# Performance work log

Measured on AMD Instinct MI355X. Metric: run time of the kernel, lower is better.

## Reference

```python
import jax, jax.numpy as jnp
import numpy as np

def setup_inputs() -> dict:
    key = jax.random.key(0)
    k0, k1, k2, k3 = jax.random.split(key, 4)
    B, L, D, E, Dg = 2, 2048, 2048, 8, 256  # Dg = D // E
    x = jax.random.normal(k0, (B, L, D), dtype=jnp.float32)
    Wg = jax.random.normal(k1, (E, D), dtype=jnp.float32) * 0.02     # gate: Linear(D, E)
    Wd = jax.random.normal(k2, (E, Dg, D), dtype=jnp.float32) * 0.02  # down: Linear(D, Dg) per expert
    Wu = jax.random.normal(k3, (E, D, Dg), dtype=jnp.float32) * 0.02  # up:   Linear(Dg, D) per expert
    return {"x": x, "Wg": Wg, "Wd": Wd, "Wu": Wu, "k": 2}

def reference(x, Wg, Wd, Wu, k):
    B, L, D = x.shape
    E = Wg.shape[0]
    T = B * L
    xf = x.reshape(T, D)
    # gate scores: sigmoid(x @ Wg^T), then top-k gate values G and expert indices I
    S = jax.nn.sigmoid(xf @ Wg.T)            # [T, E]
    G, I = jax.lax.top_k(S, k)               # [T, k], [T, k]
    # combine weights per token per expert (zero for unselected experts);
    # equivalent to the original's one_hot + per-expert gather/scatter-add.
    w = jnp.zeros((T, E), x.dtype).at[jnp.arange(T)[:, None], I].add(G)  # [T, E]
    # down: sum_e w[t,e] * (Wd[e] @ x[t])
    down = jnp.einsum('te,egd,td->tg', w, Wd, xf)   # [T, Dg]
    # inner model is identity
    # up: sum_e w[t,e] * (Wu[e] @ down[t])
    up = jnp.einsum('te,edg,tg->td', w, Wu, down)   # [T, D]
    return up.reshape(B, L, D)
```

## Files before the change

kernel.cpp:

```cpp
#include <hip/hip_runtime.h>
#include <stdint.h>

#define T_TOK 4096
#define DIM   2048
#define NEXP  8
#define DG    256
#define TOPK  2

#define BM 64
#define BN 128
#define BKU 64
#define NROWS  (T_TOK*TOPK + NEXP*BM)
#define NBLK_M (NROWS/BM)

typedef __attribute__((ext_vector_type(8))) short short8;
typedef __attribute__((ext_vector_type(4))) float f32x4;

static __device__ __forceinline__ short f2bf(float f) {
    union { float f; uint32_t u; } v{f};
    uint32_t r = v.u + 0x7fffu + ((v.u >> 16) & 1u);
    return (short)(r >> 16);
}
static __device__ __forceinline__ float b2f(short s) {
    union { uint32_t u; float f; } v{((uint32_t)(unsigned short)s) << 16};
    return v.f;
}

#define GLD16(g, l) \
    __builtin_amdgcn_global_load_lds((const __attribute__((address_space(1))) void*)(g), \
                                     (__attribute__((address_space(3))) void*)(l), 16, 0, 0)

__global__ __launch_bounds__(256) void gate_kernel(const float* __restrict__ x,
                                                   const float* __restrict__ Wg,
                                                   int* __restrict__ gidx,
                                                   float* __restrict__ gval,
                                                   short* __restrict__ x_bf)
{
    int token = blockIdx.x * 4 + (threadIdx.x >> 6);
    int lane  = threadIdx.x & 63;
    const float4* xr = (const float4*)(x + (size_t)token * DIM);

    float4 xv[8];
#pragma unroll
    for (int i = 0; i < 8; i++) xv[i] = xr[lane + 64 * i];

    short4* xb = (short4*)(x_bf + (size_t)token * DIM);
#pragma unroll
    for (int i = 0; i < 8; i++) {
        short4 o;
        o.x = f2bf(xv[i].x); o.y = f2bf(xv[i].y);
        o.z = f2bf(xv[i].z); o.w = f2bf(xv[i].w);
        xb[lane + 64 * i] = o;
    }

    float acc[NEXP];
#pragma unroll
    for (int e = 0; e < NEXP; e++) {
        const float4* wr = (const float4*)(Wg + e * DIM);
        float a = 0.0f;
#pragma unroll
        for (int i = 0; i < 8; i++) {
            float4 w = wr[lane + 64 * i];
            a += xv[i].x * w.x + xv[i].y * w.y + xv[i].z * w.z + xv[i].w * w.w;
        }
        acc[e] = a;
    }

#pragma unroll
    for (int m = 1; m < 64; m <<= 1) {
#pragma unroll
        for (int e = 0; e < NEXP; e++) acc[e] += __shfl_xor(acc[e], m, 64);
    }

    if (lane == 0) {
        float sg[NEXP];
#pragma unroll
        for (int e = 0; e < NEXP; e++) sg[e] = 1.0f / (1.0f + expf(-acc[e]));
        int i0 = 0;
#pragma unroll
        for (int e = 1; e < NEXP; e++) if (sg[e] > sg[i0]) i0 = e;
        int i1 = (i0 == 0) ? 1 : 0;
#pragma unroll
        for (int e = 0; e < NEXP; e++) if (e != i0 && e != i1 && sg[e] > sg[i1]) i1 = e;
        gidx[2 * token + 0] = i0;
        gidx[2 * token + 1] = i1;
        gval[2 * token + 0] = sg[i0];
        gval[2 * token + 1] = sg[i1];
    }
}

__global__ __launch_bounds__(256) void convW_kernel(const float* __restrict__ Wd,
                                                    const float* __restrict__ Wu,
                                                    short* __restrict__ Wd_bf,
                                                    short* __restrict__ Wu_bf,
                                                    int n4)
{
    int i = blockIdx.x * 256 + threadIdx.x;
    const float* s; short* d; int j;
    if (i < n4)      { s = Wd; d = Wd_bf; j = i; }
    else             { s = Wu; d = Wu_bf; j = i - n4; if (j >= n4) return; }
    float4 v = ((const float4*)s)[j];
    short4 o;
    o.x = f2bf(v.x); o.y = f2bf(v.y); o.z = f2bf(v.z); o.w = f2bf(v.w);
    ((short4*)d)[j] = o;
}

__global__ __launch_bounds__(1024) void bucket_kernel(const int* __restrict__ gidx,
                                                      int* __restrict__ rowtok,
                                                      int* __restrict__ rowpos,
                                                      int* __restrict__ seg_off)
{
    __shared__ int cnt[NEXP];
    __shared__ int cur[NEXP];
    int tid = threadIdx.x;
    if (tid < NEXP) cnt[tid] = 0;
    __syncthreads();

    for (int t = tid; t < T_TOK; t += 1024) {
        atomicAdd(&cnt[gidx[2 * t + 0]], 1);
        atomicAdd(&cnt[gidx[2 * t + 1]], 1);
    }
    __syncthreads();

    if (tid == 0) {
        int o = 0;
        for (int e = 0; e < NEXP; e++) {
            seg_off[e] = o;
            cur[e] = o;
            o += ((cnt[e] + BM - 1) / BM) * BM;
        }
        seg_off[NEXP] = o;
    }
    __syncthreads();

    for (int r = tid; r < NROWS; r += 1024) rowtok[r] = -1;
    __syncthreads();

    for (int t = tid; t < T_TOK; t += 1024) {
        for (int s = 0; s < TOPK; s++) {
            int e = gidx[2 * t + s];
            int p = atomicAdd(&cur[e], 1);
            rowtok[p] = t;
            rowpos[2 * t + s] = p;
        }
    }
}

#define AS3 __attribute__((address_space(3)))

#define STAGE(B_) do { \
    GLD16(agA0, lA_##B_##_0); \
    GLD16(agA1, lA_##B_##_1); \
    GLD16(agB0, lB_##B_##_0); \
    GLD16(agB1, lB_##B_##_1); \
    GLD16(agB2, lB_##B_##_2); \
    GLD16(agB3, lB_##B_##_3); \
    agA0 += BKU; agA1 += BKU; \
    agB0 += BKU; agB1 += BKU; agB2 += BKU; agB3 += BKU; \
} while (0)

#define COMP(B_) do { \
    short8 a00 = *(const short8*)&As[B_][am0][c0]; \
    short8 a10 = *(const short8*)&As[B_][am1][c0]; \
    short8 b00 = *(const short8*)&Bs[B_][bn0][c0]; \
    short8 b10 = *(const short8*)&Bs[B_][bn1][c0]; \
    short8 b20 = *(const short8*)&Bs[B_][bn2][c0]; \
    short8 b30 = *(const short8*)&Bs[B_][bn3][c0]; \
    short8 a01 = *(const short8*)&As[B_][am0][c1]; \
    short8 a11 = *(const short8*)&As[B_][am1][c1]; \
    short8 b01 = *(const short8*)&Bs[B_][bn0][c1]; \
    short8 b11 = *(const short8*)&Bs[B_][bn1][c1]; \
    short8 b21 = *(const short8*)&Bs[B_][bn2][c1]; \
    short8 b31 = *(const short8*)&Bs[B_][bn3][c1]; \
    acc[0][0] = __builtin_amdgcn_mfma_f32_16x16x32_bf16(a00, b00, acc[0][0], 0, 0, 0); \
    acc[0][1] = __builtin_amdgcn_mfma_f32_16x16x32_bf16(a00, b10, acc[0][1], 0, 0, 0); \
    acc[0][2] = __builtin_amdgcn_mfma_f32_16x16x32_bf16(a00, b20, acc[0][2], 0, 0, 0); \
    acc[0][3] = __builtin_amdgcn_mfma_f32_16x16x32_bf16(a00, b30, acc[0][3], 0, 0, 0); \
    acc[1][0] = __builtin_amdgcn_mfma_f32_16x16x32_bf16(a10, b00, acc[1][0], 0, 0, 0); \
    acc[1][1] = __builtin_amdgcn_mfma_f32_16x16x32_bf16(a10, b10, acc[1][1], 0, 0, 0); \
    acc[1][2] = __builtin_amdgcn_mfma_f32_16x16x32_bf16(a10, b20, acc[1][2], 0, 0, 0); \
    acc[1][3] = __builtin_amdgcn_mfma_f32_16x16x32_bf16(a10, b30, acc[1][3], 0, 0, 0); \
    acc[0][0] = __builtin_amdgcn_mfma_f32_16x16x32_bf16(a01, b01, acc[0][0], 0, 0, 0); \
    acc[0][1] = __builtin_amdgcn_mfma_f32_16x16x32_bf16(a01, b11, acc[0][1], 0, 0, 0); \
    acc[0][2] = __builtin_amdgcn_mfma_f32_16x16x32_bf16(a01, b21, acc[0][2], 0, 0, 0); \
    acc[0][3] = __builtin_amdgcn_mfma_f32_16x16x32_bf16(a01, b31, acc[0][3], 0, 0, 0); \
    acc[1][0] = __builtin_amdgcn_mfma_f32_16x16x32_bf16(a11, b01, acc[1][0], 0, 0, 0); \
    acc[1][1] = __builtin_amdgcn_mfma_f32_16x16x32_bf16(a11, b11, acc[1][1], 0, 0, 0); \
    acc[1][2] = __builtin_amdgcn_mfma_f32_16x16x32_bf16(a11, b21, acc[1][2], 0, 0, 0); \
    acc[1][3] = __builtin_amdgcn_mfma_f32_16x16x32_bf16(a11, b31, acc[1][3], 0, 0, 0); \
} while (0)

template<int K, int Ntot>
__global__ __launch_bounds__(256) void gemm_kernel(const short* __restrict__ A,
                                                   const short* __restrict__ B,
                                                   const int* __restrict__ rowtok,
                                                   const int* __restrict__ seg_off,
                                                   short* __restrict__ C)
{
    __shared__ __align__(16) short As[2][BM][BKU];
    __shared__ __align__(16) short Bs[2][BN][BKU];

    int row0 = blockIdx.x * BM;
    int total = seg_off[NEXP];
    if (row0 >= total) return;
    int e = 0;
    while (row0 >= seg_off[e + 1]) ++e;
    int n0 = blockIdx.y * BN;

    int tid = threadIdx.x;
    int w = tid >> 6, l = tid & 63;

    int srow = (w << 3) + (l >> 3);
    int sc   = ((l & 7) ^ ((l >> 3) & 7)) << 3;

    int ta0 = rowtok[row0 + srow];      if (ta0 < 0) ta0 = 0;
    int ta1 = rowtok[row0 + 32 + srow]; if (ta1 < 0) ta1 = 0;
    const short* agA0 = A + (size_t)ta0 * K + sc;
    const short* agA1 = A + (size_t)ta1 * K + sc;
    const short* be = B + (size_t)e * Ntot * K + (size_t)n0 * K;
    const short* agB0 = be + (size_t)(srow     ) * K + sc;
    const short* agB1 = be + (size_t)(srow + 32) * K + sc;
    const short* agB2 = be + (size_t)(srow + 64) * K + sc;
    const short* agB3 = be + (size_t)(srow + 96) * K + sc;

    auto lA_0_0 = (AS3 void*)&As[0][(w << 3)     ][0];
    auto lA_0_1 = (AS3 void*)&As[0][(w << 3) + 32][0];
    auto lA_1_0 = (AS3 void*)&As[1][(w << 3)     ][0];
    auto lA_1_1 = (AS3 void*)&As[1][(w << 3) + 32][0];
    auto lB_0_0 = (AS3 void*)&Bs[0][(w << 3)     ][0];
    auto lB_0_1 = (AS3 void*)&Bs[0][(w << 3) + 32][0];
    auto lB_0_2 = (AS3 void*)&Bs[0][(w << 3) + 64][0];
    auto lB_0_3 = (AS3 void*)&Bs[0][(w << 3) + 96][0];
    auto lB_1_0 = (AS3 void*)&Bs[1][(w << 3)     ][0];
    auto lB_1_1 = (AS3 void*)&Bs[1][(w << 3) + 32][0];
    auto lB_1_2 = (AS3 void*)&Bs[1][(w << 3) + 64][0];
    auto lB_1_3 = (AS3 void*)&Bs[1][(w << 3) + 96][0];

    int mlane = l & 15, qlane = l >> 4;
    int wm = w >> 1, wn = w & 1;
    int c0 = (qlane ^ (mlane & 7)) << 3;
    int c1 = c0 ^ 32;
    int am0 = wm * 32 + mlane, am1 = am0 + 16;
    int bn0 = wn * 64 + mlane, bn1 = bn0 + 16, bn2 = bn0 + 32, bn3 = bn0 + 48;

    f32x4 acc[2][4] = {};

    STAGE(0);
    __syncthreads();
    constexpr int NT = K / BKU;
#pragma unroll 1
    for (int t = 0; t < NT; t += 2) {
        if (t + 1 < NT) STAGE(1);
        COMP(0);
        __syncthreads();
        if (t + 2 < NT) STAGE(0);
        COMP(1);
        __syncthreads();
    }

#pragma unroll
    for (int i = 0; i < 2; i++) {
        int rbase = row0 + wm * 32 + i * 16 + qlane * 4;
#pragma unroll
        for (int j = 0; j < 4; j++) {
            int col = n0 + wn * 64 + j * 16 + mlane;
#pragma unroll
            for (int r = 0; r < 4; r++)
                C[(size_t)(rbase + r) * Ntot + col] = f2bf(acc[i][j][r]);
        }
    }
}

#undef STAGE
#undef COMP
#undef AS3

__global__ __launch_bounds__(256) void combine1_kernel(const short* __restrict__ dr,
                                                       const int* __restrict__ rowpos,
                                                       const float* __restrict__ gval,
                                                       short* __restrict__ dt)
{
    int t = blockIdx.x, d = threadIdx.x;
    int   p0 = rowpos[2 * t], p1 = rowpos[2 * t + 1];
    float g0 = gval[2 * t],   g1 = gval[2 * t + 1];
    float v = g0 * b2f(dr[(size_t)p0 * DG + d]) + g1 * b2f(dr[(size_t)p1 * DG + d]);
    dt[(size_t)t * DG + d] = f2bf(v);
}

__global__ __launch_bounds__(256) void combine2_kernel(const short* __restrict__ ur,
                                                       const int* __restrict__ rowpos,
                                                       const float* __restrict__ gval,
                                                       float* __restrict__ out)
{
    int i = blockIdx.x * 256 + threadIdx.x;
    int t = i >> 9;
    int c = (i & 511) * 4;
    int   p0 = rowpos[2 * t], p1 = rowpos[2 * t + 1];
    float g0 = gval[2 * t],   g1 = gval[2 * t + 1];
    short4 u0 = *(const short4*)&ur[(size_t)p0 * DIM + c];
    short4 u1 = *(const short4*)&ur[(size_t)p1 * DIM + c];
    float4 o;
    o.x = g0 * b2f(u0.x) + g1 * b2f(u1.x);
    o.y = g0 * b2f(u0.y) + g1 * b2f(u1.y);
    o.z = g0 * b2f(u0.z) + g1 * b2f(u1.z);
    o.w = g0 * b2f(u0.w) + g1 * b2f(u1.w);
    *(float4*)&out[(size_t)t * DIM + c] = o;
}

extern "C" void kernel_launch(void* const* d_in, const int* in_sizes, int n_in,
                              void* d_out, int out_size, void* d_ws, size_t ws_size,
                              hipStream_t stream) {
    const float* x  = (const float*)d_in[0];
    const float* Wg = (const float*)d_in[1];
    const float* Wd = (const float*)d_in[2];
    const float* Wu = (const float*)d_in[3];
    float* out = (float*)d_out;

    char* p = (char*)d_ws;
    int*   gidx    = (int*)(p + 0);
    float* gval    = (float*)(p + 32768);
    int*   rowtok  = (int*)(p + 65536);
    int*   rowpos  = (int*)(p + 100352);
    int*   seg_off = (int*)(p + 133120);
    short* x_bf    = (short*)(p + 133376);
    short* Wd_bf   = (short*)(p + 133376 + 16777216);
    short* Wu_bf   = Wd_bf + 4194304;
    short* dr_bf   = Wu_bf + 4194304;
    short* dt_bf   = dr_bf + (size_t)NROWS * DG;
    short* ur_bf   = dt_bf + (size_t)T_TOK * DG;

    const int W4 = NEXP * DG * DIM / 4;
    gate_kernel<<<T_TOK / 4, 256, 0, stream>>>(x, Wg, gidx, gval, x_bf);
    convW_kernel<<<(2 * W4 + 255) / 256, 256, 0, stream>>>(Wd, Wu, Wd_bf, Wu_bf, W4);
    bucket_kernel<<<1, 1024, 0, stream>>>(gidx, rowtok, rowpos, seg_off);

    gemm_kernel<DIM, DG><<<dim3(NBLK_M, DG / BN), 256, 0, stream>>>(x_bf, Wd_bf, rowtok, seg_off, dr_bf);
    combine1_kernel<<<T_TOK, 256, 0, stream>>>(dr_bf, rowpos, gval, dt_bf);
    gemm_kernel<DG, DIM><<<dim3(NBLK_M, DIM / BN), 256, 0, stream>>>(dt_bf, Wu_bf, rowtok, seg_off, ur_bf);
    combine2_kernel<<<T_TOK * DIM / 4 / 256, 256, 0, stream>>>(ur_bf, rowpos, gval, out);
}
```

Measured before the change: 197.0 us.

## Deepen GEMM prefetch with vmcnt waits and use wave-aggregated bucket atomics

The GEMM main loop now issues two stages of global-to-LDS loads up front. It waits with explicit s_waitcnt vmcnt counts plus raw barriers instead of full __syncthreads, so one stage's loads stay in flight while the other stage is computed. Separately, the bucket kernel replaces per-token LDS atomics with wave ballots and popcounts, doing one atomic per expert per wave. The aim is to hide global load latency and cut atomic contention. The risk is relying on exact vmcnt accounting being correct, and the odd/even tail handling assumes NT is even.

```diff
diff --git a/kernel.cpp b/kernel.cpp
--- a/kernel.cpp
+++ b/kernel.cpp
@@ -112,14 +112,25 @@
 {
     __shared__ int cnt[NEXP];
     __shared__ int cur[NEXP];
-    int tid = threadIdx.x;
+    int tid = threadIdx.x, lane = tid & 63;
     if (tid < NEXP) cnt[tid] = 0;
     __syncthreads();
 
-    for (int t = tid; t < T_TOK; t += 1024) {
-        atomicAdd(&cnt[gidx[2 * t + 0]], 1);
-        atomicAdd(&cnt[gidx[2 * t + 1]], 1);
-    }
+    int e_[8];
+#pragma unroll
+    for (int r = 0; r < 8; r++) e_[r] = gidx[r * 1024 + tid];
+
+    int mycnt = 0;
+#pragma unroll
+    for (int r = 0; r < 8; r++) {
+        int e = e_[r];
+#pragma unroll
+        for (int ee = 0; ee < NEXP; ee++) {
+            unsigned long long m = __ballot(e == ee);
+            if (lane == ee) mycnt += (int)__popcll(m);
+        }
+    }
+    if (lane < NEXP) atomicAdd(&cnt[lane], mycnt);
     __syncthreads();
 
     if (tid == 0) {
@@ -136,17 +147,31 @@
     for (int r = tid; r < NROWS; r += 1024) rowtok[r] = -1;
     __syncthreads();
 
-    for (int t = tid; t < T_TOK; t += 1024) {
-        for (int s = 0; s < TOPK; s++) {
-            int e = gidx[2 * t + s];
-            int p = atomicAdd(&cur[e], 1);
-            rowtok[p] = t;
-            rowpos[2 * t + s] = p;
+#pragma unroll
+    for (int r = 0; r < 8; r++) {
+        int idx = r * 1024 + tid;
+        int e = e_[r];
+#pragma unroll
+        for (int ee = 0; ee < NEXP; ee++) {
+            unsigned long long m = __ballot(e == ee);
+            if (m == 0) continue;
+            int leader = __ffsll((unsigned long long)m) - 1;
+            int base = 0;
+            if (lane == leader) base = atomicAdd(&cur[ee], (int)__popcll(m));
+            base = __shfl(base, leader, 64);
+            if (e == ee) {
+                int pos = base + (int)__popcll(m & ((1ull << lane) - 1ull));
+                rowtok[pos] = idx >> 1;
+                rowpos[idx] = pos;
+            }
         }
     }
 }
 
 #define AS3 __attribute__((address_space(3)))
+
+#define VMCNT(N) asm volatile("s_waitcnt vmcnt(" #N ")" ::: "memory")
+#define BAR()    __builtin_amdgcn_s_barrier()
 
 #define STAGE(B_) do { \
     GLD16(agA0, lA_##B_##_0); \
@@ -245,18 +270,25 @@
 
     f32x4 acc[2][4] = {};
 
+    constexpr int NT = K / BKU;
     STAGE(0);
-    __syncthreads();
-    constexpr int NT = K / BKU;
+    STAGE(1);
 #pragma unroll 1
-    for (int t = 0; t < NT; t += 2) {
-        if (t + 1 < NT) STAGE(1);
+    for (int t = 0; t < NT - 2; t += 2) {
+        VMCNT(6); BAR();
         COMP(0);
-        __syncthreads();
-        if (t + 2 < NT) STAGE(0);
+        BAR();
+        STAGE(0);
+        VMCNT(6); BAR();
         COMP(1);
-        __syncthreads();
-    }
+        BAR();
+        if (t + 3 < NT) STAGE(1);
+    }
+    VMCNT(6); BAR();
+    COMP(0);
+    BAR();
+    VMCNT(0); BAR();
+    COMP(1);
 
 #pragma unroll
     for (int i = 0; i < 2; i++) {
```

Result: slower. 204.9 us (+4.0%).
